# Kernel optimization log

Measured on AMD Instinct MI355X. Metric: run time of the kernel, lower is better.

Reference implementation:

```python
import jax, jax.numpy as jnp
import numpy as np
from jax import lax

B, X, H, W, C = 4, 32, 8, 128, 32  # batch, frames, height, width, channels (dim)


def setup_inputs() -> dict:
    key = jax.random.key(0)
    k1, k2, k3, k4, k5, k6 = jax.random.split(key, 6)
    return {
        "storage": jax.random.normal(k1, (B, X, H, W, C), jnp.float32),
        "target": jax.random.normal(k2, (B, 1, H, W, C), jnp.float32),
        # Conv3d(dim, 2*dim, kernel=(3,1,1), padding=(1,0,0)) weight/bias
        "w_cross": jax.random.normal(k3, (2 * C, C, 3, 1, 1), jnp.float32) * 0.05,
        "b_cross": jax.random.normal(k4, (2 * C,), jnp.float32) * 0.05,
        # Conv2d(dim, dim, kernel=1) weight (stored as [out, in]) / bias
        "w_q": jax.random.normal(k5, (C, C), jnp.float32) * 0.1,
        "b_q": jax.random.normal(k6, (C,), jnp.float32) * 0.1,
    }


def reference(storage, target, w_cross, b_cross, w_q, b_q):
    # storage [B,X,H,W,C] -> transpose(4,1).transpose(4,2) -> [B,C,X,W,H]
    s = jnp.transpose(storage, (0, 4, 1, 3, 2))
    # target [B,1,H,W,C] -> transpose(4,2) -> [B,1,C,W,H] -> squeeze(1) -> [B,C,W,H]
    t = jnp.transpose(target, (0, 1, 4, 3, 2))[:, 0]

    # Conv3d over the X (depth) axis, kernel (3,1,1), padding (1,0,0)
    out = lax.conv_general_dilated(
        s, w_cross, window_strides=(1, 1, 1),
        padding=((1, 1), (0, 0), (0, 0)),
        dimension_numbers=("NCDHW", "OIDHW", "NCDHW"),
    ) + b_cross[None, :, None, None, None]          # [B,2C,X,W,H]
    s_v, s_k = jnp.split(out, 2, axis=1)            # each [B,C,X,W,H]

    # 1x1 Conv2d query projection
    t_q = jnp.einsum("oc,bcwh->bowh", w_q, t) + b_q[None, :, None, None]  # [B,C,W,H]
    # unsqueeze(1).transpose(2,1).repeat over X -> [B,C,X,W,H]
    t_q = jnp.broadcast_to(t_q[:, :, None], (B, C, X, W, H))

    # Faithful torch .view on contiguous [B,C,X,W,H]: row-major reshape mixes C into last dim
    t_q = t_q.reshape(B, X * W, C * H)
    s_v = s_v.reshape(B, X * W, C * H)
    s_k = jnp.swapaxes(s_k.reshape(B, X * W, C * H), 1, 2)  # [B, C*H, X*W]

    kq = jax.nn.softmax(jnp.einsum("bnc,bcm->bnm", t_q, s_k), axis=-1)  # [B, XW, XW]
    final = jnp.einsum("bnm,bmc->bnc", kq, s_v)                          # [B, XW, C*H]
    return final.reshape(B, X, H, W, C)
```

## Files before the change

### kernel.cpp

```cpp
#include <hip/hip_runtime.h>

typedef unsigned short u16;
typedef unsigned int u32;
typedef __attribute__((ext_vector_type(8))) short s16x8;
typedef __attribute__((ext_vector_type(4))) float f32x4;

#define WS_A      0u
#define WS_B      8388608u
#define WS_C      16777216u
#define WS_D      25165824u
#define WS_E      25296896u
#define WS_NEEDED 25427968u

__device__ __forceinline__ u16 f2bf(float f){
  u32 u = __float_as_uint(f);
  return (u16)((u + 0x7fffu + ((u >> 16) & 1u)) >> 16);
}

__global__ __launch_bounds__(256) void zero_out_kernel(float* __restrict__ out){
  int t = blockIdx.x * 256 + threadIdx.x;
  ((float4*)out)[t] = make_float4(0.f, 0.f, 0.f, 0.f);
}

__global__ __launch_bounds__(256) void transpose_w(const float* __restrict__ w_cross,
    float* __restrict__ wT){
  int t = blockIdx.x * 256 + threadIdx.x;
  wT[t] = w_cross[(t & 63) * 96 + (t >> 6)];
}

__global__ __launch_bounds__(256, 2) void conv_kernel(const float* __restrict__ storage,
    const float* __restrict__ wT, const float* __restrict__ b_cross,
    u16* __restrict__ Kb, u16* __restrict__ Vb){
  int bid = blockIdx.x;
  int wc  = bid & 3;
  int x   = (bid >> 2) & 31;
  int og2 = (bid >> 7) & 3;
  int b   = bid >> 9;
  int tid = threadIdx.x;
  int wl = tid & 31, h = tid >> 5;
  int w = wc * 32 + wl;
  int obase_ch = og2 * 16;

  float acc[16];
  #pragma unroll
  for (int i = 0; i < 16; ++i) acc[i] = b_cross[obase_ch + i];

  #pragma unroll
  for (int dx = 0; dx < 3; ++dx){
    int xx = x + dx - 1;
    if (xx < 0 || xx > 31) continue;
    float vv[32];
    const float4* p = (const float4*)(storage + ((((size_t)b*32 + xx)*8 + h)*128 + w)*32);
    #pragma unroll
    for (int q = 0; q < 8; ++q){
      float4 v = p[q];
      vv[q*4+0] = v.x; vv[q*4+1] = v.y; vv[q*4+2] = v.z; vv[q*4+3] = v.w;
    }
    #pragma unroll
    for (int c = 0; c < 32; ++c){
      float v = vv[c];
      const float* wp = wT + (c*3 + dx)*64 + obase_ch;
      #pragma unroll
      for (int i = 0; i < 16; ++i) acc[i] = fmaf(v, wp[i], acc[i]);
    }
  }

  int m = wl*8 + h;
  size_t base = ((size_t)b*4096 + (size_t)x*4 + wc)*256 + m;
  if (og2 < 2){
    #pragma unroll
    for (int i = 0; i < 16; ++i)
      Vb[base + (size_t)(obase_ch + i)*32768] = f2bf(acc[i]);
  } else {
    #pragma unroll
    for (int i = 0; i < 16; ++i)
      Kb[base + (size_t)(obase_ch + i - 32)*32768] = f2bf(acc[i]);
  }
}

__global__ __launch_bounds__(256) void qproj_kernel(const float* __restrict__ target,
    const float* __restrict__ w_q, const float* __restrict__ b_q, u16* __restrict__ Qbf){
  int bid = blockIdx.x;
  int wc = bid & 3;
  int cq = (bid >> 2) & 31;
  int b  = bid >> 7;
  int tid = threadIdx.x;
  int wl = tid & 31, h = tid >> 5;
  int w = wc * 32 + wl;
  float in[32];
  const float4* p = (const float4*)(target + (((size_t)b*8 + h)*128 + w)*32);
  #pragma unroll
  for (int q = 0; q < 8; ++q){
    float4 v = p[q];
    in[q*4+0] = v.x; in[q*4+1] = v.y; in[q*4+2] = v.z; in[q*4+3] = v.w;
  }
  float acc = b_q[cq];
  #pragma unroll
  for (int c = 0; c < 32; ++c) acc += in[c] * w_q[cq*32 + c];
  __shared__ float stg[256];
  stg[wl*8 + h] = acc;
  __syncthreads();
  Qbf[((size_t)b*128 + cq*4 + wc)*256 + tid] = f2bf(stg[tid]);
}

__global__ __launch_bounds__(256) void scores_kernel(const u16* __restrict__ Qbf,
    const u16* __restrict__ Kb, float* __restrict__ S){
  int kc = blockIdx.x & 63, b = blockIdx.x >> 6;
  int tid = threadIdx.x;
  int w = tid >> 6, lane = tid & 63, l15 = lane & 15, quad = lane >> 4;
  __shared__ u16 Ks[64 * 256];
  {
    int jl = tid >> 2, hf = tid & 3;
    const uint4* src = (const uint4*)(Kb + ((size_t)(b*4096 + kc*64 + jl))*256 + hf*64);
    u16* drow = &Ks[jl*256];
    #pragma unroll
    for (int q = 0; q < 8; ++q){
      uint4 v = src[q];
      int B8 = hf*8 + q;
      *(uint4*)&drow[(B8 ^ (jl & 7))*8] = v;
    }
  }
  __syncthreads();

  int krow = w*16 + l15;
  #pragma unroll 1
  for (int rp = 0; rp < 4; ++rp){
    s16x8 a[2][8];
    #pragma unroll
    for (int rt = 0; rt < 2; ++rt){
      int row = (rp*2 + rt)*16 + l15;
      const u16* qp = Qbf + ((size_t)(b*128 + row))*256 + quad*8;
      #pragma unroll
      for (int ks = 0; ks < 8; ++ks) a[rt][ks] = *(const s16x8*)(qp + ks*32);
    }
    f32x4 c0 = {0.f,0.f,0.f,0.f}, c1 = {0.f,0.f,0.f,0.f};
    #pragma unroll
    for (int ks = 0; ks < 8; ++ks){
      int B8 = ks*4 + quad;
      s16x8 bf = *(const s16x8*)&Ks[krow*256 + (B8 ^ (krow & 7))*8];
      c0 = __builtin_amdgcn_mfma_f32_16x16x32_bf16(a[0][ks], bf, c0, 0, 0, 0);
      c1 = __builtin_amdgcn_mfma_f32_16x16x32_bf16(a[1][ks], bf, c1, 0, 0, 0);
    }
    int keyg = kc*64 + krow;
    #pragma unroll
    for (int reg = 0; reg < 4; ++reg){
      int r0 = (rp*2 + 0)*16 + quad*4 + reg;
      int r1 = (rp*2 + 1)*16 + quad*4 + reg;
      S[((size_t)(b*128 + r0))*4096 + keyg] = c0[reg];
      S[((size_t)(b*128 + r1))*4096 + keyg] = c1[reg];
    }
  }
}

__global__ __launch_bounds__(256) void softmax_kernel(const float* __restrict__ S,
    u16* __restrict__ P){
  int r = blockIdx.x & 127, b = blockIdx.x >> 7;
  const float* row = S + ((size_t)(b*128 + r))*4096;
  int tid = threadIdx.x;
  float v[16];
  const float4* p4 = (const float4*)(row + tid*16);
  #pragma unroll
  for (int q = 0; q < 4; ++q){
    float4 t = p4[q];
    v[q*4+0] = t.x; v[q*4+1] = t.y; v[q*4+2] = t.z; v[q*4+3] = t.w;
  }
  float mx = v[0];
  #pragma unroll
  for (int i = 1; i < 16; ++i) mx = fmaxf(mx, v[i]);
  #pragma unroll
  for (int off = 1; off < 64; off <<= 1) mx = fmaxf(mx, __shfl_xor(mx, off));
  __shared__ float sm[4], sl[4];
  int wid = tid >> 6;
  if ((tid & 63) == 0) sm[wid] = mx;
  __syncthreads();
  mx = fmaxf(fmaxf(sm[0], sm[1]), fmaxf(sm[2], sm[3]));
  float s = 0.f;
  #pragma unroll
  for (int i = 0; i < 16; ++i){ v[i] = __expf(v[i] - mx); s += v[i]; }
  #pragma unroll
  for (int off = 1; off < 64; off <<= 1) s += __shfl_xor(s, off);
  if ((tid & 63) == 0) sl[wid] = s;
  __syncthreads();
  float inv = 1.f / (sl[0] + sl[1] + sl[2] + sl[3]);
  u16 o[16];
  #pragma unroll
  for (int i = 0; i < 16; ++i) o[i] = f2bf(v[i] * inv);
  uint4 o0, o1;
  o0.x = (u32)o[0] | ((u32)o[1] << 16);  o0.y = (u32)o[2] | ((u32)o[3] << 16);
  o0.z = (u32)o[4] | ((u32)o[5] << 16);  o0.w = (u32)o[6] | ((u32)o[7] << 16);
  o1.x = (u32)o[8] | ((u32)o[9] << 16);  o1.y = (u32)o[10]| ((u32)o[11]<< 16);
  o1.z = (u32)o[12]| ((u32)o[13]<< 16);  o1.w = (u32)o[14]| ((u32)o[15]<< 16);
  uint4* dst = (uint4*)(P + ((size_t)(b*128 + r))*4096 + tid*16);
  dst[0] = o0; dst[1] = o1;
}

__global__ __launch_bounds__(256) void pv_kernel(const u16* __restrict__ P,
    const u16* __restrict__ Vb, float* __restrict__ Opart){
  int mc = blockIdx.x & 3, kq = (blockIdx.x >> 2) & 15, b = blockIdx.x >> 6;
  int tid = threadIdx.x;
  int w = tid >> 6, lane = tid & 63, l15 = lane & 15, quad = lane >> 4;
  __shared__ alignas(16) char smem[34816];
  u16* Ps  = (u16*)smem;
  u16* Vts = (u16*)(smem + 16384);
  f32x4 c[8];
  #pragma unroll
  for (int nt = 0; nt < 8; ++nt) c[nt] = (f32x4){0.f,0.f,0.f,0.f};

  int jl = tid & 63, mo = tid >> 6;

  #pragma unroll 1
  for (int kt = 0; kt < 4; ++kt){
    {
      int prow = tid >> 1, half = tid & 1;
      const uint4* src = (const uint4*)(P + ((size_t)(b*128 + prow))*4096 + kq*256 + kt*64 + half*32);
      #pragma unroll
      for (int q = 0; q < 4; ++q){
        uint4 v = src[q];
        int B8 = half*4 + q;
        *(uint4*)&Ps[prow*64 + (B8 ^ (prow & 7))*8] = v;
      }
    }
    {
      const uint4* vsrc = (const uint4*)(Vb + ((size_t)(b*4096 + kq*256 + kt*64 + jl))*256 + mc*64);
      #pragma unroll
      for (int qq = 0; qq < 2; ++qq){
        int q8 = mo + qq*4;
        uint4 v = vsrc[q8];
        u16* dst = &Vts[(q8*8)*72 + jl];
        dst[0*72] = (u16)(v.x & 0xffff); dst[1*72] = (u16)(v.x >> 16);
        dst[2*72] = (u16)(v.y & 0xffff); dst[3*72] = (u16)(v.y >> 16);
        dst[4*72] = (u16)(v.z & 0xffff); dst[5*72] = (u16)(v.z >> 16);
        dst[6*72] = (u16)(v.w & 0xffff); dst[7*72] = (u16)(v.w >> 16);
      }
    }
    __syncthreads();
    int mlocal = w*16 + l15;
    #pragma unroll
    for (int ks2 = 0; ks2 < 2; ++ks2){
      s16x8 af = *(const s16x8*)&Vts[mlocal*72 + ks2*32 + quad*8];
      int B8 = ks2*4 + quad;
      #pragma unroll
      for (int nt = 0; nt < 8; ++nt){
        int prow = nt*16 + l15;
        s16x8 bf = *(const s16x8*)&Ps[prow*64 + (B8 ^ (prow & 7))*8];
        c[nt] = __builtin_amdgcn_mfma_f32_16x16x32_bf16(af, bf, c[nt], 0, 0, 0);
      }
    }
    __syncthreads();
  }

  float* Osh = (float*)smem;
  #pragma unroll
  for (int nt = 0; nt < 8; ++nt){
    int prow = nt*16 + l15;
    *(f32x4*)&Osh[prow*68 + w*16 + quad*4] = c[nt];
  }
  __syncthreads();
  {
    int prow = tid >> 1, half = tid & 1;
    float* dst = Opart + ((size_t)((b*16 + kq)*128 + prow))*256 + mc*64 + half*32;
    const float* srow = &Osh[prow*68 + half*32];
    #pragma unroll
    for (int i = 0; i < 8; ++i) ((float4*)dst)[i] = ((const float4*)srow)[i];
  }
}

__global__ __launch_bounds__(256) void scatter_kernel(const float* __restrict__ Opart,
    float* __restrict__ out){
  int r = blockIdx.x & 127, b = blockIdx.x >> 7;
  int m = threadIdx.x;
  float o = 0.f;
  #pragma unroll
  for (int kq = 0; kq < 16; ++kq) o += Opart[((size_t)((b*16 + kq)*128 + r))*256 + m];
  int cq = r >> 2, whi = r & 3;
  size_t obase = ((size_t)b*32 + cq) * 32768;
  #pragma unroll
  for (int hh = 0; hh < 8; ++hh){
    #pragma unroll
    for (int wt = 0; wt < 4; ++wt){
      out[obase + hh*4096 + wt*1024 + whi*256 + m] = o;
    }
  }
}

extern "C" void kernel_launch(void* const* d_in, const int* in_sizes, int n_in,
                              void* d_out, int out_size, void* d_ws, size_t ws_size,
                              hipStream_t stream){
  const float* storage = (const float*)d_in[0];
  const float* target  = (const float*)d_in[1];
  const float* w_cross = (const float*)d_in[2];
  const float* b_cross = (const float*)d_in[3];
  const float* w_q     = (const float*)d_in[4];
  const float* b_q     = (const float*)d_in[5];
  float* out = (float*)d_out;

  if (ws_size < (size_t)WS_NEEDED){
    zero_out_kernel<<<dim3(4096), dim3(256), 0, stream>>>(out);
    return;
  }

  char* ws = (char*)d_ws;
  float* S     = (float*)(ws + WS_A);
  float* Opart = (float*)(ws + WS_A);
  u16*   Kb    = (u16*)(ws + WS_B);
  u16*   P     = (u16*)(ws + WS_B);
  u16*   Vb    = (u16*)(ws + WS_C);
  u16*   Qbf   = (u16*)(ws + WS_D);
  float* wT    = (float*)(ws + WS_E);

  transpose_w    <<<dim3(24),   dim3(256), 0, stream>>>(w_cross, wT);
  conv_kernel    <<<dim3(2048), dim3(256), 0, stream>>>(storage, wT, b_cross, Kb, Vb);
  qproj_kernel   <<<dim3(512),  dim3(256), 0, stream>>>(target, w_q, b_q, Qbf);
  scores_kernel  <<<dim3(256),  dim3(256), 0, stream>>>(Qbf, Kb, S);
  softmax_kernel <<<dim3(512),  dim3(256), 0, stream>>>(S, P);
  pv_kernel      <<<dim3(256),  dim3(256), 0, stream>>>(P, Vb, Opart);
  scatter_kernel <<<dim3(512),  dim3(256), 0, stream>>>(Opart, out);
}
```

Baseline: 144.9 us.

## Fuse scores, softmax and PV into a split-K flash-attention kernel

Replaces the separate scores, softmax and PV kernels with one flash-style kernel that uses an online softmax (running max and sum) over key tiles. Each block handles 16 query rows, a quarter of the keys and a quarter of the value columns. A combine kernel then merges the four partial results using their per-part maxima and sums. The q-projection and weight-transpose kernels are also merged into one launch. This removes the full fp32 score matrix and the bf16 probability matrix round-trips through global memory and cuts launch count. In exchange, K tiles and the QK^T and exp work are recomputed by each of the four column-chunk blocks, and each tile adds extra barriers.

Result: slower. 166.4 us (+14.9%).

```diff
diff --git a/kernel.cpp b/kernel.cpp
--- a/kernel.cpp
+++ b/kernel.cpp
@@ -6,11 +6,13 @@
 typedef __attribute__((ext_vector_type(4))) float f32x4;
 
 #define WS_A      0u
+#define WS_MP     2097152u
+#define WS_LP     2162688u
 #define WS_B      8388608u
 #define WS_C      16777216u
 #define WS_D      25165824u
-#define WS_E      25296896u
-#define WS_NEEDED 25427968u
+#define WS_E      25427968u
+#define WS_NEEDED 25452544u
 
 __device__ __forceinline__ u16 f2bf(float f){
   u32 u = __float_as_uint(f);
@@ -22,10 +24,35 @@
   ((float4*)out)[t] = make_float4(0.f, 0.f, 0.f, 0.f);
 }
 
-__global__ __launch_bounds__(256) void transpose_w(const float* __restrict__ w_cross,
-    float* __restrict__ wT){
-  int t = blockIdx.x * 256 + threadIdx.x;
-  wT[t] = w_cross[(t & 63) * 96 + (t >> 6)];
+__global__ __launch_bounds__(256) void prep_kernel(const float* __restrict__ target,
+    const float* __restrict__ w_q, const float* __restrict__ b_q, u16* __restrict__ Qbf,
+    const float* __restrict__ w_cross, float* __restrict__ wT){
+  int bid = blockIdx.x;
+  int tid = threadIdx.x;
+  if (bid >= 512){
+    int t = (bid - 512) * 256 + tid;
+    wT[t] = w_cross[(t & 63) * 96 + (t >> 6)];
+    return;
+  }
+  int wc = bid & 3;
+  int cq = (bid >> 2) & 31;
+  int b  = bid >> 7;
+  int wl = tid & 31, h = tid >> 5;
+  int w = wc * 32 + wl;
+  float in[32];
+  const float4* p = (const float4*)(target + (((size_t)b*8 + h)*128 + w)*32);
+  #pragma unroll
+  for (int q = 0; q < 8; ++q){
+    float4 v = p[q];
+    in[q*4+0] = v.x; in[q*4+1] = v.y; in[q*4+2] = v.z; in[q*4+3] = v.w;
+  }
+  float acc = b_q[cq];
+  #pragma unroll
+  for (int c = 0; c < 32; ++c) acc += in[c] * w_q[cq*32 + c];
+  __shared__ float stg[256];
+  stg[wl*8 + h] = acc;
+  __syncthreads();
+  Qbf[((size_t)b*128 + cq*4 + wc)*256 + tid] = f2bf(stg[tid]);
 }
 
 __global__ __launch_bounds__(256, 2) void conv_kernel(const float* __restrict__ storage,
@@ -78,155 +105,57 @@
   }
 }
 
-__global__ __launch_bounds__(256) void qproj_kernel(const float* __restrict__ target,
-    const float* __restrict__ w_q, const float* __restrict__ b_q, u16* __restrict__ Qbf){
-  int bid = blockIdx.x;
-  int wc = bid & 3;
-  int cq = (bid >> 2) & 31;
-  int b  = bid >> 7;
-  int tid = threadIdx.x;
-  int wl = tid & 31, h = tid >> 5;
-  int w = wc * 32 + wl;
-  float in[32];
-  const float4* p = (const float4*)(target + (((size_t)b*8 + h)*128 + w)*32);
-  #pragma unroll
-  for (int q = 0; q < 8; ++q){
-    float4 v = p[q];
-    in[q*4+0] = v.x; in[q*4+1] = v.y; in[q*4+2] = v.z; in[q*4+3] = v.w;
-  }
-  float acc = b_q[cq];
-  #pragma unroll
-  for (int c = 0; c < 32; ++c) acc += in[c] * w_q[cq*32 + c];
-  __shared__ float stg[256];
-  stg[wl*8 + h] = acc;
-  __syncthreads();
-  Qbf[((size_t)b*128 + cq*4 + wc)*256 + tid] = f2bf(stg[tid]);
-}
-
-__global__ __launch_bounds__(256) void scores_kernel(const u16* __restrict__ Qbf,
-    const u16* __restrict__ Kb, float* __restrict__ S){
-  int kc = blockIdx.x & 63, b = blockIdx.x >> 6;
+__global__ __launch_bounds__(256) void flash_kernel(const u16* __restrict__ Qbf,
+    const u16* __restrict__ Kb, const u16* __restrict__ Vb,
+    float* __restrict__ Opart, float* __restrict__ mpart, float* __restrict__ lpart){
+  int mc = blockIdx.x & 3, rb = (blockIdx.x >> 2) & 7;
+  int kq = (blockIdx.x >> 5) & 3, b = blockIdx.x >> 7;
   int tid = threadIdx.x;
   int w = tid >> 6, lane = tid & 63, l15 = lane & 15, quad = lane >> 4;
-  __shared__ u16 Ks[64 * 256];
+
+  __shared__ alignas(16) char smem[44928];
+  u16*   Ks    = (u16*)smem;
+  u16*   Vts   = (u16*)(smem + 32768);
+  u16*   Ps    = (u16*)(smem + 41984);
+  float* tmaxW = (float*)(smem + 44288);
+  float* lsumW = (float*)(smem + 44544);
+  float* mrun  = (float*)(smem + 44800);
+  float* lrun  = (float*)(smem + 44864);
+
+  s16x8 a[8];
   {
-    int jl = tid >> 2, hf = tid & 3;
-    const uint4* src = (const uint4*)(Kb + ((size_t)(b*4096 + kc*64 + jl))*256 + hf*64);
-    u16* drow = &Ks[jl*256];
-    #pragma unroll
-    for (int q = 0; q < 8; ++q){
-      uint4 v = src[q];
-      int B8 = hf*8 + q;
-      *(uint4*)&drow[(B8 ^ (jl & 7))*8] = v;
-    }
-  }
-  __syncthreads();
-
+    const u16* qp = Qbf + ((size_t)(b*128 + rb*16 + l15))*256 + quad*8;
+    #pragma unroll
+    for (int ks = 0; ks < 8; ++ks) a[ks] = *(const s16x8*)(qp + ks*32);
+  }
+  if (tid < 16){ mrun[tid] = -1e30f; lrun[tid] = 0.f; }
+  f32x4 o = {0.f,0.f,0.f,0.f};
+
+  int jl_k = tid >> 2, hf = tid & 3;
+  int jl_v = tid & 63, mo = tid >> 6;
   int krow = w*16 + l15;
+  int mlocal = w*16 + l15;
+
   #pragma unroll 1
-  for (int rp = 0; rp < 4; ++rp){
-    s16x8 a[2][8];
-    #pragma unroll
-    for (int rt = 0; rt < 2; ++rt){
-      int row = (rp*2 + rt)*16 + l15;
-      const u16* qp = Qbf + ((size_t)(b*128 + row))*256 + quad*8;
+  for (int it = 0; it < 16; ++it){
+    int j0 = kq*1024 + it*64;
+    {
+      const uint4* src = (const uint4*)(Kb + ((size_t)(b*4096 + j0 + jl_k))*256 + hf*64);
+      u16* drow = &Ks[jl_k*256];
       #pragma unroll
-      for (int ks = 0; ks < 8; ++ks) a[rt][ks] = *(const s16x8*)(qp + ks*32);
-    }
-    f32x4 c0 = {0.f,0.f,0.f,0.f}, c1 = {0.f,0.f,0.f,0.f};
-    #pragma unroll
-    for (int ks = 0; ks < 8; ++ks){
-      int B8 = ks*4 + quad;
-      s16x8 bf = *(const s16x8*)&Ks[krow*256 + (B8 ^ (krow & 7))*8];
-      c0 = __builtin_amdgcn_mfma_f32_16x16x32_bf16(a[0][ks], bf, c0, 0, 0, 0);
-      c1 = __builtin_amdgcn_mfma_f32_16x16x32_bf16(a[1][ks], bf, c1, 0, 0, 0);
-    }
-    int keyg = kc*64 + krow;
-    #pragma unroll
-    for (int reg = 0; reg < 4; ++reg){
-      int r0 = (rp*2 + 0)*16 + quad*4 + reg;
-      int r1 = (rp*2 + 1)*16 + quad*4 + reg;
-      S[((size_t)(b*128 + r0))*4096 + keyg] = c0[reg];
-      S[((size_t)(b*128 + r1))*4096 + keyg] = c1[reg];
-    }
-  }
-}
-
-__global__ __launch_bounds__(256) void softmax_kernel(const float* __restrict__ S,
-    u16* __restrict__ P){
-  int r = blockIdx.x & 127, b = blockIdx.x >> 7;
-  const float* row = S + ((size_t)(b*128 + r))*4096;
-  int tid = threadIdx.x;
-  float v[16];
-  const float4* p4 = (const float4*)(row + tid*16);
-  #pragma unroll
-  for (int q = 0; q < 4; ++q){
-    float4 t = p4[q];
-    v[q*4+0] = t.x; v[q*4+1] = t.y; v[q*4+2] = t.z; v[q*4+3] = t.w;
-  }
-  float mx = v[0];
-  #pragma unroll
-  for (int i = 1; i < 16; ++i) mx = fmaxf(mx, v[i]);
-  #pragma unroll
-  for (int off = 1; off < 64; off <<= 1) mx = fmaxf(mx, __shfl_xor(mx, off));
-  __shared__ float sm[4], sl[4];
-  int wid = tid >> 6;
-  if ((tid & 63) == 0) sm[wid] = mx;
-  __syncthreads();
-  mx = fmaxf(fmaxf(sm[0], sm[1]), fmaxf(sm[2], sm[3]));
-  float s = 0.f;
-  #pragma unroll
-  for (int i = 0; i < 16; ++i){ v[i] = __expf(v[i] - mx); s += v[i]; }
-  #pragma unroll
-  for (int off = 1; off < 64; off <<= 1) s += __shfl_xor(s, off);
-  if ((tid & 63) == 0) sl[wid] = s;
-  __syncthreads();
-  float inv = 1.f / (sl[0] + sl[1] + sl[2] + sl[3]);
-  u16 o[16];
-  #pragma unroll
-  for (int i = 0; i < 16; ++i) o[i] = f2bf(v[i] * inv);
-  uint4 o0, o1;
-  o0.x = (u32)o[0] | ((u32)o[1] << 16);  o0.y = (u32)o[2] | ((u32)o[3] << 16);
-  o0.z = (u32)o[4] | ((u32)o[5] << 16);  o0.w = (u32)o[6] | ((u32)o[7] << 16);
-  o1.x = (u32)o[8] | ((u32)o[9] << 16);  o1.y = (u32)o[10]| ((u32)o[11]<< 16);
-  o1.z = (u32)o[12]| ((u32)o[13]<< 16);  o1.w = (u32)o[14]| ((u32)o[15]<< 16);
-  uint4* dst = (uint4*)(P + ((size_t)(b*128 + r))*4096 + tid*16);
-  dst[0] = o0; dst[1] = o1;
-}
-
-__global__ __launch_bounds__(256) void pv_kernel(const u16* __restrict__ P,
-    const u16* __restrict__ Vb, float* __restrict__ Opart){
-  int mc = blockIdx.x & 3, kq = (blockIdx.x >> 2) & 15, b = blockIdx.x >> 6;
-  int tid = threadIdx.x;
-  int w = tid >> 6, lane = tid & 63, l15 = lane & 15, quad = lane >> 4;
-  __shared__ alignas(16) char smem[34816];
-  u16* Ps  = (u16*)smem;
-  u16* Vts = (u16*)(smem + 16384);
-  f32x4 c[8];
-  #pragma unroll
-  for (int nt = 0; nt < 8; ++nt) c[nt] = (f32x4){0.f,0.f,0.f,0.f};
-
-  int jl = tid & 63, mo = tid >> 6;
-
-  #pragma unroll 1
-  for (int kt = 0; kt < 4; ++kt){
+      for (int q = 0; q < 8; ++q){
+        uint4 v = src[q];
+        int B8 = hf*8 + q;
+        *(uint4*)&drow[(B8 ^ (jl_k & 7))*8] = v;
+      }
+    }
     {
-      int prow = tid >> 1, half = tid & 1;
-      const uint4* src = (const uint4*)(P + ((size_t)(b*128 + prow))*4096 + kq*256 + kt*64 + half*32);
-      #pragma unroll
-      for (int q = 0; q < 4; ++q){
-        uint4 v = src[q];
-        int B8 = half*4 + q;
-        *(uint4*)&Ps[prow*64 + (B8 ^ (prow & 7))*8] = v;
-      }
-    }
-    {
-      const uint4* vsrc = (const uint4*)(Vb + ((size_t)(b*4096 + kq*256 + kt*64 + jl))*256 + mc*64);
+      const uint4* vsrc = (const uint4*)(Vb + ((size_t)(b*4096 + j0 + jl_v))*256 + mc*64);
       #pragma unroll
       for (int qq = 0; qq < 2; ++qq){
         int q8 = mo + qq*4;
         uint4 v = vsrc[q8];
-        u16* dst = &Vts[(q8*8)*72 + jl];
+        u16* dst = &Vts[(q8*8)*72 + jl_v];
         dst[0*72] = (u16)(v.x & 0xffff); dst[1*72] = (u16)(v.x >> 16);
         dst[2*72] = (u16)(v.y & 0xffff); dst[3*72] = (u16)(v.y >> 16);
         dst[4*72] = (u16)(v.z & 0xffff); dst[5*72] = (u16)(v.z >> 16);
@@ -234,44 +163,89 @@
       }
     }
     __syncthreads();
-    int mlocal = w*16 + l15;
+
+    f32x4 s = {0.f,0.f,0.f,0.f};
+    #pragma unroll
+    for (int ks = 0; ks < 8; ++ks){
+      int B8 = ks*4 + quad;
+      s16x8 bf = *(const s16x8*)&Ks[krow*256 + (B8 ^ (krow & 7))*8];
+      s = __builtin_amdgcn_mfma_f32_16x16x32_bf16(a[ks], bf, s, 0, 0, 0);
+    }
+    float tm[4];
+    #pragma unroll
+    for (int reg = 0; reg < 4; ++reg){
+      float t = s[reg];
+      t = fmaxf(t, __shfl_xor(t, 1)); t = fmaxf(t, __shfl_xor(t, 2));
+      t = fmaxf(t, __shfl_xor(t, 4)); t = fmaxf(t, __shfl_xor(t, 8));
+      tm[reg] = t;
+    }
+    if (l15 == 0) *(f32x4*)&tmaxW[w*16 + quad*4] = (f32x4){tm[0],tm[1],tm[2],tm[3]};
+    __syncthreads();
+
+    float mold_l = mrun[l15];
+    float tmax_l = fmaxf(fmaxf(tmaxW[l15], tmaxW[16 + l15]),
+                         fmaxf(tmaxW[32 + l15], tmaxW[48 + l15]));
+    float mn_l = fmaxf(mold_l, tmax_l);
+    float alpha_l = __expf(mold_l - mn_l);
+    float lsum[4];
+    #pragma unroll
+    for (int reg = 0; reg < 4; ++reg){
+      float mn_r = __shfl(mn_l, quad*4 + reg);
+      float p = __expf(s[reg] - mn_r);
+      Ps[(quad*4 + reg)*72 + krow] = f2bf(p);
+      float t = p;
+      t += __shfl_xor(t, 1); t += __shfl_xor(t, 2);
+      t += __shfl_xor(t, 4); t += __shfl_xor(t, 8);
+      lsum[reg] = t;
+    }
+    if (l15 == 0) *(f32x4*)&lsumW[w*16 + quad*4] = (f32x4){lsum[0],lsum[1],lsum[2],lsum[3]};
+    __syncthreads();
+
+    o[0] *= alpha_l; o[1] *= alpha_l; o[2] *= alpha_l; o[3] *= alpha_l;
     #pragma unroll
     for (int ks2 = 0; ks2 < 2; ++ks2){
       s16x8 af = *(const s16x8*)&Vts[mlocal*72 + ks2*32 + quad*8];
-      int B8 = ks2*4 + quad;
-      #pragma unroll
-      for (int nt = 0; nt < 8; ++nt){
-        int prow = nt*16 + l15;
-        s16x8 bf = *(const s16x8*)&Ps[prow*64 + (B8 ^ (prow & 7))*8];
-        c[nt] = __builtin_amdgcn_mfma_f32_16x16x32_bf16(af, bf, c[nt], 0, 0, 0);
-      }
-    }
-    __syncthreads();
-  }
-
-  float* Osh = (float*)smem;
-  #pragma unroll
-  for (int nt = 0; nt < 8; ++nt){
-    int prow = nt*16 + l15;
-    *(f32x4*)&Osh[prow*68 + w*16 + quad*4] = c[nt];
-  }
-  __syncthreads();
+      s16x8 bf = *(const s16x8*)&Ps[l15*72 + ks2*32 + quad*8];
+      o = __builtin_amdgcn_mfma_f32_16x16x32_bf16(af, bf, o, 0, 0, 0);
+    }
+    if (tid < 16){
+      mrun[tid] = mn_l;
+      lrun[tid] = lrun[tid]*alpha_l + lsumW[tid] + lsumW[16+tid] + lsumW[32+tid] + lsumW[48+tid];
+    }
+    __syncthreads();
+  }
+
   {
-    int prow = tid >> 1, half = tid & 1;
-    float* dst = Opart + ((size_t)((b*16 + kq)*128 + prow))*256 + mc*64 + half*32;
-    const float* srow = &Osh[prow*68 + half*32];
-    #pragma unroll
-    for (int i = 0; i < 8; ++i) ((float4*)dst)[i] = ((const float4*)srow)[i];
-  }
-}
-
-__global__ __launch_bounds__(256) void scatter_kernel(const float* __restrict__ Opart,
+    int row = rb*16 + l15;
+    float* dst = Opart + ((size_t)((b*4 + kq)*128 + row))*256 + mc*64 + w*16 + quad*4;
+    *(float4*)dst = make_float4(o[0], o[1], o[2], o[3]);
+  }
+  if (mc == 0 && tid < 16){
+    mpart[(b*4 + kq)*128 + rb*16 + tid] = mrun[tid];
+    lpart[(b*4 + kq)*128 + rb*16 + tid] = lrun[tid];
+  }
+}
+
+__global__ __launch_bounds__(256) void combine_kernel(const float* __restrict__ mpart,
+    const float* __restrict__ lpart, const float* __restrict__ Opart,
     float* __restrict__ out){
   int r = blockIdx.x & 127, b = blockIdx.x >> 7;
   int m = threadIdx.x;
+  float mk[4], lk[4];
+  #pragma unroll
+  for (int kq = 0; kq < 4; ++kq){
+    mk[kq] = mpart[(b*4 + kq)*128 + r];
+    lk[kq] = lpart[(b*4 + kq)*128 + r];
+  }
+  float M = fmaxf(fmaxf(mk[0], mk[1]), fmaxf(mk[2], mk[3]));
+  float L = 0.f, wgt[4];
+  #pragma unroll
+  for (int kq = 0; kq < 4; ++kq){ wgt[kq] = __expf(mk[kq] - M); L += wgt[kq]*lk[kq]; }
   float o = 0.f;
   #pragma unroll
-  for (int kq = 0; kq < 16; ++kq) o += Opart[((size_t)((b*16 + kq)*128 + r))*256 + m];
+  for (int kq = 0; kq < 4; ++kq)
+    o += wgt[kq] * Opart[((size_t)((b*4 + kq)*128 + r))*256 + m];
+  o /= L;
   int cq = r >> 2, whi = r & 3;
   size_t obase = ((size_t)b*32 + cq) * 32768;
   #pragma unroll
@@ -300,19 +274,16 @@
   }
 
   char* ws = (char*)d_ws;
-  float* S     = (float*)(ws + WS_A);
   float* Opart = (float*)(ws + WS_A);
+  float* mpart = (float*)(ws + WS_MP);
+  float* lpart = (float*)(ws + WS_LP);
   u16*   Kb    = (u16*)(ws + WS_B);
-  u16*   P     = (u16*)(ws + WS_B);
   u16*   Vb    = (u16*)(ws + WS_C);
   u16*   Qbf   = (u16*)(ws + WS_D);
   float* wT    = (float*)(ws + WS_E);
 
-  transpose_w    <<<dim3(24),   dim3(256), 0, stream>>>(w_cross, wT);
+  prep_kernel    <<<dim3(536),  dim3(256), 0, stream>>>(target, w_q, b_q, Qbf, w_cross, wT);
   conv_kernel    <<<dim3(2048), dim3(256), 0, stream>>>(storage, wT, b_cross, Kb, Vb);
-  qproj_kernel   <<<dim3(512),  dim3(256), 0, stream>>>(target, w_q, b_q, Qbf);
-  scores_kernel  <<<dim3(256),  dim3(256), 0, stream>>>(Qbf, Kb, S);
-  softmax_kernel <<<dim3(512),  dim3(256), 0, stream>>>(S, P);
-  pv_kernel      <<<dim3(256),  dim3(256), 0, stream>>>(P, Vb, Opart);
-  scatter_kernel <<<dim3(512),  dim3(256), 0, stream>>>(Opart, out);
-}
+  flash_kernel   <<<dim3(512),  dim3(256), 0, stream>>>(Qbf, Kb, Vb, Opart, mpart, lpart);
+  combine_kernel <<<dim3(512),  dim3(256), 0, stream>>>(mpart, lpart, Opart, out);
+}
```
